# Performance work log

Hardware: AMD Instinct MI355X
Metric: run time of the kernel (lower is better)

## Reference

```python
import jax, jax.numpy as jnp
import numpy as np

B, T, C = 1, 4096, 1024
NH, NKV, HD = 16, 4, 64
N_REP = NH // NKV
WIN = 1024
EPS = 1e-5
ROPE_THETA = 10000.0


def setup_inputs() -> dict:
    key = jax.random.key(0)
    ks = jax.random.split(key, 6)
    s = 1.0 / np.sqrt(C)
    x = jax.random.normal(ks[0], (B, T, C), jnp.float32)
    wq = jax.random.normal(ks[1], (NH * HD, C), jnp.float32) * s
    wk = jax.random.normal(ks[2], (NKV * HD, C), jnp.float32) * s
    wv = jax.random.normal(ks[3], (NKV * HD, C), jnp.float32) * s
    wo = jax.random.normal(ks[4], (C, NH * HD), jnp.float32) * (1.0 / np.sqrt(NH * HD))
    q_norm_w = jnp.ones((HD,), jnp.float32)
    k_norm_w = jnp.ones((HD,), jnp.float32)
    # RoPE tables: (T, HD//2)
    inv_freq = 1.0 / (ROPE_THETA ** (np.arange(0, HD, 2, dtype=np.float32) / HD))
    ang = np.outer(np.arange(T, dtype=np.float32), inv_freq)
    freqs_cos = jnp.asarray(np.cos(ang), jnp.float32)
    freqs_sin = jnp.asarray(np.sin(ang), jnp.float32)
    return {"x": x, "wq": wq, "wk": wk, "wv": wv, "wo": wo,
            "q_norm_w": q_norm_w, "k_norm_w": k_norm_w,
            "freqs_cos": freqs_cos, "freqs_sin": freqs_sin}


def _rmsnorm(v, w):
    # RMSNorm over last dim (per-head)
    return v * jax.lax.rsqrt(jnp.mean(v * v, axis=-1, keepdims=True) + EPS) * w


def _rope(v, cos, sin):
    # v: (B, T, H, HD); interleaved complex rotation, matching torch polar freqs_cis
    vr, vi = v[..., 0::2], v[..., 1::2]
    c = cos[None, :, None, :]
    s = sin[None, :, None, :]
    out_r = vr * c - vi * s
    out_i = vr * s + vi * c
    return jnp.stack([out_r, out_i], axis=-1).reshape(v.shape)


def reference(x, wq, wk, wv, wo, q_norm_w, k_norm_w, freqs_cos, freqs_sin):
    xq = jnp.einsum('btc,dc->btd', x, wq).reshape(B, T, NH, HD)
    xk = jnp.einsum('btc,dc->btd', x, wk).reshape(B, T, NKV, HD)
    xv = jnp.einsum('btc,dc->btd', x, wv).reshape(B, T, NKV, HD)
    # per-head QK RMSNorm
    xq = _rmsnorm(xq, q_norm_w)
    xk = _rmsnorm(xk, k_norm_w)
    # RoPE
    xq = _rope(xq, freqs_cos, freqs_sin)
    xk = _rope(xk, freqs_cos, freqs_sin)
    # GQA: expand kv heads
    xk = jnp.repeat(xk, N_REP, axis=2)  # (B, T, NH, HD)
    xv = jnp.repeat(xv, N_REP, axis=2)
    scale = 1.0 / np.sqrt(HD)
    scores = jnp.einsum('bthd,bshd->bhts', xq, xk) * scale
    i = jnp.arange(T)[:, None]
    j = jnp.arange(T)[None, :]
    mask = (i >= j) & (i - j < WIN)  # causal + sliding window
    scores = jnp.where(mask[None, None], scores, -jnp.inf)
    attn = jax.nn.softmax(scores, axis=-1)
    y = jnp.einsum('bhts,bshd->bthd', attn, xv).reshape(B, T, NH * HD)
    return jnp.einsum('btd,cd->btc', y, wo)
```

## Files before the change

### kernel.cpp

```cpp
#include <hip/hip_runtime.h>
#include <hip/hip_bf16.h>


#define WIN_SZ 1024

typedef __attribute__((ext_vector_type(8))) short short8;
typedef __attribute__((ext_vector_type(8))) unsigned short ushort8;
typedef __attribute__((ext_vector_type(4))) float f32x4;
typedef __attribute__((ext_vector_type(16))) float f32x16;

#define GLOAD_LDS16(g, s)                                              \
  __builtin_amdgcn_global_load_lds(                                    \
      (const __attribute__((address_space(1))) unsigned int*)(g),      \
      (__attribute__((address_space(3))) unsigned int*)(s), 16, 0, 0)

__device__ __forceinline__ unsigned short f2bf(float f) {
  union { float f; unsigned u; } v; v.f = f;
  unsigned r = v.u + 0x7fffu + ((v.u >> 16) & 1u);
  return (unsigned short)(r >> 16);
}

__device__ __forceinline__ unsigned pk2bf(float lo, float hi) {
  __hip_bfloat162 h = __float22bfloat162_rn(make_float2(lo, hi));
  union { __hip_bfloat162 h; unsigned u; } c; c.h = h; return c.u;
}

__device__ __forceinline__ short8 frag4(unsigned w0, unsigned w1, unsigned w2, unsigned w3) {
  union { unsigned u[4]; short8 s; } x;
  x.u[0] = w0; x.u[1] = w1; x.u[2] = w2; x.u[3] = w3; return x.s;
}

__global__ __launch_bounds__(256) void k_f2b_all(const float* __restrict__ x,
                                                 const float* __restrict__ wq,
                                                 const float* __restrict__ wk,
                                                 const float* __restrict__ wv,
                                                 const float* __restrict__ wo,
                                                 unsigned short* __restrict__ xb,
                                                 unsigned short* __restrict__ wqkvb,
                                                 unsigned short* __restrict__ wob) {
  int q = blockIdx.x * 256 + threadIdx.x;
  const float* src;
  unsigned short* dst;
  int off;
  if (q < 1048576) { src = x; dst = xb; off = q; }
  else if (q < 1310720) { src = wq; dst = wqkvb; off = q - 1048576; }
  else if (q < 1376256) { src = wk; dst = wqkvb + 1024 * 1024; off = q - 1310720; }
  else if (q < 1441792) { src = wv; dst = wqkvb + 1280 * 1024; off = q - 1376256; }
  else { src = wo; dst = wob; off = q - 1441792; }
  float4 v = ((const float4*)src)[off];
  ushort4 o;
  o.x = f2bf(v.x); o.y = f2bf(v.y); o.z = f2bf(v.z); o.w = f2bf(v.w);
  ((ushort4*)dst)[off] = o;
}

__global__ __launch_bounds__(256) void k_gemm_qkv(const unsigned short* __restrict__ A,
                                                  const unsigned short* __restrict__ B,
                                                  const float* __restrict__ qw,
                                                  const float* __restrict__ kw,
                                                  const float* __restrict__ fc,
                                                  const float* __restrict__ fs,
                                                  unsigned short* __restrict__ Qb,
                                                  unsigned short* __restrict__ Kb,
                                                  unsigned short* __restrict__ Vtg) {
  const int K = 1024;
  __shared__ unsigned short As[2][128 * 64];
  __shared__ unsigned short Bs[2][64 * 64];
  const int id = blockIdx.x;
  const int chunk = gridDim.x >> 3;
  const int swz = (id & 7) * chunk + (id >> 3);
  const int n_idx = swz % 24, m_idx = swz / 24;
  const int m0 = m_idx * 128, n0 = n_idx * 64;

  const int tid = threadIdx.x;
  const int w = tid >> 6, l = tid & 63;
  const int wr = w >> 1, wc = w & 1;
  const int r = l & 15, g = l >> 4;
  const int lr = l >> 3, lc = l & 7;
  const int srowb = w * 32, browb = w * 16;

  f32x4 acc[4][2];
#pragma unroll
  for (int i = 0; i < 4; i++)
#pragma unroll
    for (int j = 0; j < 2; j++) acc[i][j] = {0.f, 0.f, 0.f, 0.f};

  const unsigned short* Ag = A + (size_t)(m0 + srowb + lr) * K + lc * 8;
  const unsigned short* Bg = B + (size_t)(n0 + browb + lr) * K + lc * 8;

  auto stage = [&](int buf, int k0) {
#pragma unroll
    for (int it = 0; it < 4; it++)
      GLOAD_LDS16(Ag + (size_t)(it * 8) * K + k0, &As[buf][(srowb + it * 8) * 64]);
#pragma unroll
    for (int it = 0; it < 2; it++)
      GLOAD_LDS16(Bg + (size_t)(it * 8) * K + k0, &Bs[buf][(browb + it * 8) * 64]);
  };

  stage(0, 0);
  __syncthreads();
  int cur = 0;
  const int NT = K >> 6;
  for (int t = 0; t < NT; ++t) {
    if (t + 1 < NT) stage(cur ^ 1, (t + 1) << 6);
    const char* Ab = (const char*)As[cur];
    const char* Bb = (const char*)Bs[cur];
#pragma unroll
    for (int kk = 0; kk < 2; kk++) {
      short8 af[4], bfr[2];
#pragma unroll
      for (int mi = 0; mi < 4; mi++)
        af[mi] = *(const short8*)(Ab + (wr * 64 + mi * 16 + r) * 128 + kk * 64 + g * 16);
#pragma unroll
      for (int nj = 0; nj < 2; nj++)
        bfr[nj] = *(const short8*)(Bb + (wc * 32 + nj * 16 + r) * 128 + kk * 64 + g * 16);
#pragma unroll
      for (int mi = 0; mi < 4; mi++)
#pragma unroll
        for (int nj = 0; nj < 2; nj++)
          acc[mi][nj] = __builtin_amdgcn_mfma_f32_16x16x32_bf16(af[mi], bfr[nj], acc[mi][nj], 0, 0, 0);
    }
    __syncthreads();
    cur ^= 1;
  }

  const int u = n0 >> 6;
  if (u < 20) {
    float* ssb = (float*)As;
    f32x4 sv[4];
#pragma unroll
    for (int mi = 0; mi < 4; mi++) {
      f32x4 s;
#pragma unroll
      for (int e = 0; e < 4; e++)
        s[e] = acc[mi][0][e] * acc[mi][0][e] + acc[mi][1][e] * acc[mi][1][e];
#pragma unroll
      for (int off = 1; off < 16; off <<= 1)
#pragma unroll
        for (int e = 0; e < 4; e++) s[e] += __shfl_xor(s[e], off);
      sv[mi] = s;
    }
    if (r == 0) {
#pragma unroll
      for (int mi = 0; mi < 4; mi++)
#pragma unroll
        for (int e = 0; e < 4; e++)
          ssb[(wr * 64 + mi * 16 + g * 4 + e) * 2 + wc] = sv[mi][e];
    }
    __syncthreads();
    const float escale = (u < 16) ? 0.1803368801111204f : 1.0f;
    const float* wgt = (u < 16) ? qw : kw;
#pragma unroll
    for (int mi = 0; mi < 4; mi++) {
      const int rl0 = wr * 64 + mi * 16 + g * 4;
      const int row0 = m0 + rl0;
#pragma unroll
      for (int e = 0; e < 4; e++) {
        const int row = row0 + e;
        float ss = ssb[(rl0 + e) * 2] + ssb[(rl0 + e) * 2 + 1];
        float rms = rsqrtf(ss * (1.0f / 64.0f) + 1e-5f);
#pragma unroll
        for (int nj = 0; nj < 2; nj++) {
          const int cl = wc * 32 + nj * 16 + r;
          float vn = acc[mi][nj][e] * rms * wgt[cl];
          float c = fc[row * 32 + (cl >> 1)];
          float s = fs[row * 32 + (cl >> 1)];
          float pvn = __shfl_xor(vn, 1);
          float outv = (cl & 1) ? (pvn * s + vn * c) : (vn * c - pvn * s);
          unsigned short ob = f2bf(outv * escale);
          if (u < 16) Qb[(size_t)row * 1024 + n0 + cl] = ob;
          else Kb[(size_t)row * 256 + (n0 - 1024) + cl] = ob;
        }
      }
    }
  } else {
#pragma unroll
    for (int mi = 0; mi < 4; mi++) {
      const int row0 = m0 + wr * 64 + mi * 16 + g * 4;
#pragma unroll
      for (int nj = 0; nj < 2; nj++) {
        const int d = (n0 - 1280) + wc * 32 + nj * 16 + r;
        ushort4 ov;
        ov.x = f2bf(acc[mi][nj][0]);
        ov.y = f2bf(acc[mi][nj][1]);
        ov.z = f2bf(acc[mi][nj][2]);
        ov.w = f2bf(acc[mi][nj][3]);
        *(ushort4*)(Vtg + (size_t)d * 4096 + row0) = ov;
      }
    }
  }
}

__global__ __launch_bounds__(256) void k_gemm_out(const unsigned short* __restrict__ A,
                                                  const unsigned short* __restrict__ B,
                                                  float* __restrict__ C) {
  const int K = 1024, N = 1024;
  __shared__ unsigned short As[2][128 * 64];
  __shared__ unsigned short Bs[2][64 * 64];
  const int id = blockIdx.x;
  const int chunk = gridDim.x >> 3;
  const int swz = (id & 7) * chunk + (id >> 3);
  const int n_idx = swz % 16, m_idx = swz / 16;
  const int m0 = m_idx * 128, n0 = n_idx * 64;

  const int tid = threadIdx.x;
  const int w = tid >> 6, l = tid & 63;
  const int wr = w >> 1, wc = w & 1;
  const int r = l & 15, g = l >> 4;
  const int lr = l >> 3, lc = l & 7;
  const int srowb = w * 32, browb = w * 16;

  f32x4 acc[4][2];
#pragma unroll
  for (int i = 0; i < 4; i++)
#pragma unroll
    for (int j = 0; j < 2; j++) acc[i][j] = {0.f, 0.f, 0.f, 0.f};

  const unsigned short* Ag = A + (size_t)(m0 + srowb + lr) * K + lc * 8;
  const unsigned short* Bg = B + (size_t)(n0 + browb + lr) * K + lc * 8;

  auto stage = [&](int buf, int k0) {
#pragma unroll
    for (int it = 0; it < 4; it++)
      GLOAD_LDS16(Ag + (size_t)(it * 8) * K + k0, &As[buf][(srowb + it * 8) * 64]);
#pragma unroll
    for (int it = 0; it < 2; it++)
      GLOAD_LDS16(Bg + (size_t)(it * 8) * K + k0, &Bs[buf][(browb + it * 8) * 64]);
  };

  stage(0, 0);
  __syncthreads();
  int cur = 0;
  const int NT = K >> 6;
  for (int t = 0; t < NT; ++t) {
    if (t + 1 < NT) stage(cur ^ 1, (t + 1) << 6);
    const char* Ab = (const char*)As[cur];
    const char* Bb = (const char*)Bs[cur];
#pragma unroll
    for (int kk = 0; kk < 2; kk++) {
      short8 af[4], bfr[2];
#pragma unroll
      for (int mi = 0; mi < 4; mi++)
        af[mi] = *(const short8*)(Ab + (wr * 64 + mi * 16 + r) * 128 + kk * 64 + g * 16);
#pragma unroll
      for (int nj = 0; nj < 2; nj++)
        bfr[nj] = *(const short8*)(Bb + (wc * 32 + nj * 16 + r) * 128 + kk * 64 + g * 16);
#pragma unroll
      for (int mi = 0; mi < 4; mi++)
#pragma unroll
        for (int nj = 0; nj < 2; nj++)
          acc[mi][nj] = __builtin_amdgcn_mfma_f32_16x16x32_bf16(af[mi], bfr[nj], acc[mi][nj], 0, 0, 0);
    }
    __syncthreads();
    cur ^= 1;
  }

#pragma unroll
  for (int mi = 0; mi < 4; mi++)
#pragma unroll
    for (int nj = 0; nj < 2; nj++) {
      int row = m0 + wr * 64 + mi * 16 + g * 4;
      int col = n0 + wc * 32 + nj * 16 + r;
#pragma unroll
      for (int e = 0; e < 4; e++)
        C[(size_t)(row + e) * N + col] = acc[mi][nj][e];
    }
}

__global__ __launch_bounds__(512, 4) void k_attn9(const unsigned short* __restrict__ Qb,
                                                  const unsigned short* __restrict__ Kb,
                                                  const unsigned short* __restrict__ Vtg,
                                                  unsigned short* __restrict__ Yb) {
  __shared__ char smem[4 * 8192 + 1024];
  char* stage = smem;
  float* Obuf = (float*)smem;
  float* ml = (float*)(smem + 32768);

  const int id = blockIdx.x;
  const int cupair = id & 255, sel = id >> 8;
  int qi = cupair >> 1;
  if (sel) qi = 127 - qi;
  const int hk = (cupair & 1) * 2 + sel;
  const int q0 = qi * 32;

  const int tid = threadIdx.x, w = tid >> 6, l = tid & 63;
  const int hh = w & 3, half = w >> 2;
  const int h = hk * 4 + hh;
  const int l31 = l & 31, hi = l >> 5, l15 = l & 15;
  const int qrow = q0 + l31;

  int jlo = q0 - (WIN_SZ - 1);
  if (jlo < 0) jlo = 0;
  jlo &= ~63;
  const int jlast = ((q0 + 31) >> 6) << 6;
  const int nt = ((jlast - jlo) >> 6) + 1;
  const int nh0 = (nt + 1) >> 1;

  const int sb = tid >> 7;
  const int su = tid & 127;
  const int srow = su >> 1;
  const int sg = (su & 1) * 4;
  const int sbase = sb * 8192 + (srow & 31) * 256;
  const int srx = (srow & 15) << 4;
  const int srh = (srow >> 5) * 128;
  const bool isV = sb & 1;
  const unsigned short* gK = Kb + (size_t)srow * 256 + hk * 64 + sg * 8;
  const unsigned short* gV = Vtg + (size_t)(hk * 64 + srow) * 4096 + sg * 8;

  short8 qf[4];
#pragma unroll
  for (int ks = 0; ks < 4; ks++)
    qf[ks] = *(const short8*)(Qb + (size_t)qrow * 1024 + h * 64 + ks * 16 + hi * 8);

  const short8 ones = frag4(0x3F803F80u, 0x3F803F80u, 0x3F803F80u, 0x3F803F80u);

  f32x16 accO0, accO1;
#pragma unroll
  for (int i = 0; i < 16; i++) { accO0[i] = 0.f; accO1[i] = 0.f; }
  float m = -1e30f, lsum = 0.f;

  ushort8 pre[4];
  auto prefetch = [&](int s) {
    int jt0 = jlo + (s << 6);
    int t1 = nh0 + s;
    int jt1 = (t1 < nt) ? (jlo + (t1 << 6)) : jlo;
    int jt = (sb >= 2) ? jt1 : jt0;
    if (!isV) {
      const unsigned short* g = gK + (size_t)jt * 256;
#pragma unroll
      for (int e = 0; e < 4; e++) pre[e] = *(const ushort8*)(g + e * 8);
    } else {
      const unsigned short* g = gV + jt;
#pragma unroll
      for (int e = 0; e < 4; e++) pre[e] = *(const ushort8*)(g + e * 8);
    }
  };
  prefetch(0);

  const int kbase = half * 16384;
  const int vbase = kbase + 8192;

  for (int s = 0; s < nh0; ++s) {
    __syncthreads();
#pragma unroll
    for (int e = 0; e < 4; e++) {
      int dst = sbase + ((srh + (sg + e) * 16) ^ srx);
      *(ushort8*)(stage + dst) = pre[e];
    }
    __syncthreads();
    if (s + 1 < nh0) prefetch(s + 1);

    const int myt = half ? (nh0 + s) : s;
    if (myt < nt) {
      const int jt = jlo + (myt << 6);

      f32x16 st0, st1;
#pragma unroll
      for (int i = 0; i < 16; i++) { st0[i] = 0.f; st1[i] = 0.f; }
      __builtin_amdgcn_s_setprio(1);
#pragma unroll
      for (int ks = 0; ks < 4; ks++) {
        int colb = ks * 32 + hi * 16;
        short8 kf0 = *(const short8*)(stage + kbase + l31 * 256 + (colb ^ (l15 << 4)));
        st0 = __builtin_amdgcn_mfma_f32_32x32x16_bf16(kf0, qf[ks], st0, 0, 0, 0);
        short8 kf1 = *(const short8*)(stage + kbase + l31 * 256 + ((128 + colb) ^ (l15 << 4)));
        st1 = __builtin_amdgcn_mfma_f32_32x32x16_bf16(kf1, qf[ks], st1, 0, 0, 0);
      }
      __builtin_amdgcn_s_setprio(0);

      if (jt + 63 > q0 || (q0 + 31) - jt >= WIN_SZ) {
        const int jb = jt + hi * 4;
#pragma unroll
        for (int rg = 0; rg < 16; rg++) {
          int j0 = jb + (rg & 3) + 8 * (rg >> 2);
          if (!((j0 <= qrow) && (qrow - j0 < WIN_SZ))) st0[rg] = -3.0e38f;
          int j1 = j0 + 32;
          if (!((j1 <= qrow) && (qrow - j1 < WIN_SZ))) st1[rg] = -3.0e38f;
        }
      }

      float mx = st0[0];
#pragma unroll
      for (int rg = 1; rg < 16; rg++) mx = fmaxf(mx, st0[rg]);
#pragma unroll
      for (int rg = 0; rg < 16; rg++) mx = fmaxf(mx, st1[rg]);
      mx = fmaxf(mx, __shfl_xor(mx, 32));
      if (!__all(mx <= m + 8.0f)) {
        float mnew = fmaxf(m, mx);
        float alpha = exp2f(m - mnew);
#pragma unroll
        for (int rg = 0; rg < 16; rg++) { accO0[rg] *= alpha; accO1[rg] *= alpha; }
        lsum *= alpha;
        m = mnew;
      }
#pragma unroll
      for (int rg = 0; rg < 16; rg++) st0[rg] = exp2f(st0[rg] - m);
#pragma unroll
      for (int rg = 0; rg < 16; rg++) st1[rg] = exp2f(st1[rg] - m);

      unsigned pd0[2][4], pd1[2][4];
#pragma unroll
      for (int b = 0; b < 4; b++) {
        pd0[0][b] = pk2bf(st0[4 * b], st0[4 * b + 1]);
        pd1[0][b] = pk2bf(st0[4 * b + 2], st0[4 * b + 3]);
        pd0[1][b] = pk2bf(st1[4 * b], st1[4 * b + 1]);
        pd1[1][b] = pk2bf(st1[4 * b + 2], st1[4 * b + 3]);
      }

      f32x16 accL;
#pragma unroll
      for (int i = 0; i < 16; i++) accL[i] = 0.f;

      __builtin_amdgcn_s_setprio(1);
#pragma unroll
      for (int jj = 0; jj < 2; jj++) {
#pragma unroll
        for (int ks2 = 0; ks2 < 2; ks2++) {
          unsigned a0 = pd0[jj][2 * ks2], a1 = pd0[jj][2 * ks2 + 1];
          unsigned b0 = pd1[jj][2 * ks2], b1 = pd1[jj][2 * ks2 + 1];
          unsigned a0x = __shfl_xor(a0, 32), a1x = __shfl_xor(a1, 32);
          unsigned b0x = __shfl_xor(b0, 32), b1x = __shfl_xor(b1, 32);
          unsigned w0 = hi ? a1x : a0;
          unsigned w1 = hi ? b1x : b0;
          unsigned w2 = hi ? a1 : a0x;
          unsigned w3 = hi ? b1 : b0x;
          short8 pf = frag4(w0, w1, w2, w3);
          int colb2 = jj * 64 + ks2 * 32 + hi * 16;
          short8 vf0 = *(const short8*)(stage + vbase + l31 * 256 + (colb2 ^ (l15 << 4)));
          accO0 = __builtin_amdgcn_mfma_f32_32x32x16_bf16(vf0, pf, accO0, 0, 0, 0);
          short8 vf1 = *(const short8*)(stage + vbase + l31 * 256 + ((128 + colb2) ^ (l15 << 4)));
          accO1 = __builtin_amdgcn_mfma_f32_32x32x16_bf16(vf1, pf, accO1, 0, 0, 0);
          accL = __builtin_amdgcn_mfma_f32_32x32x16_bf16(ones, pf, accL, 0, 0, 0);
        }
      }
      __builtin_amdgcn_s_setprio(0);
      lsum += accL[0];
    }
  }

  __syncthreads();
  if (half == 1) {
#pragma unroll
    for (int dd = 0; dd < 2; dd++) {
      const f32x16& a = dd ? accO1 : accO0;
#pragma unroll
      for (int rg = 0; rg < 16; rg++) {
        int d = dd * 32 + 8 * (rg >> 2) + 4 * hi + (rg & 3);
        Obuf[(hh * 64 + d) * 32 + l31] = a[rg];
      }
    }
    if (!hi) { ml[(hh * 2 + 0) * 32 + l31] = m; ml[(hh * 2 + 1) * 32 + l31] = lsum; }
  }
  __syncthreads();
  if (half == 0) {
    float m1 = ml[(hh * 2 + 0) * 32 + l31];
    float l1 = ml[(hh * 2 + 1) * 32 + l31];
    float ms = fmaxf(m, m1);
    float a0 = exp2f(m - ms), a1 = exp2f(m1 - ms);
    float inv = 1.0f / (lsum * a0 + l1 * a1);
    a0 *= inv; a1 *= inv;
#pragma unroll
    for (int dd = 0; dd < 2; dd++) {
      const f32x16& a = dd ? accO1 : accO0;
#pragma unroll
      for (int b = 0; b < 4; b++) {
        float o[4];
#pragma unroll
        for (int e = 0; e < 4; e++) {
          int d = dd * 32 + 8 * b + 4 * hi + e;
          o[e] = a[4 * b + e] * a0 + Obuf[(hh * 64 + d) * 32 + l31] * a1;
        }
        union { unsigned uu[2]; ushort4 v; } ov;
        ov.uu[0] = pk2bf(o[0], o[1]);
        ov.uu[1] = pk2bf(o[2], o[3]);
        *(ushort4*)(Yb + (size_t)qrow * 1024 + h * 64 + dd * 32 + b * 8 + hi * 4) = ov.v;
      }
    }
  }
}

extern "C" void kernel_launch(void* const* d_in, const int* in_sizes, int n_in,
                              void* d_out, int out_size, void* d_ws, size_t ws_size,
                              hipStream_t stream) {
  const float* x = (const float*)d_in[0];
  const float* wq = (const float*)d_in[1];
  const float* wk = (const float*)d_in[2];
  const float* wv = (const float*)d_in[3];
  const float* wo = (const float*)d_in[4];
  const float* qw = (const float*)d_in[5];
  const float* kw = (const float*)d_in[6];
  const float* fc = (const float*)d_in[7];
  const float* fs = (const float*)d_in[8];
  float* out = (float*)d_out;

  char* p = (char*)d_ws;
  auto alloc = [&](size_t b) {
    char* q = p;
    p += (b + 255) & ~(size_t)255;
    return q;
  };
  unsigned short* xb = (unsigned short*)alloc((size_t)4096 * 1024 * 2);
  unsigned short* wqkvb = (unsigned short*)alloc((size_t)1536 * 1024 * 2);
  unsigned short* wob = (unsigned short*)alloc((size_t)1024 * 1024 * 2);
  unsigned short* Qb = (unsigned short*)alloc((size_t)4096 * 1024 * 2);
  unsigned short* Kb = (unsigned short*)alloc((size_t)4096 * 256 * 2);
  unsigned short* Vtg = (unsigned short*)alloc((size_t)256 * 4096 * 2);
  unsigned short* Yb = (unsigned short*)alloc((size_t)4096 * 1024 * 2);

  k_f2b_all<<<6656, 256, 0, stream>>>(x, wq, wk, wv, wo, xb, wqkvb, wob);
  k_gemm_qkv<<<768, 256, 0, stream>>>(xb, wqkvb, qw, kw, fc, fs, Qb, Kb, Vtg);
  k_attn9<<<512, 512, 0, stream>>>(Qb, Kb, Vtg, Yb);
  k_gemm_out<<<512, 256, 0, stream>>>(Yb, wob, out);
}
```

Baseline: 108.8 us.

## Stage two K/V tiles per barrier pair in sliding-window attention kernel

The attention kernel now stages two 64-key K/V tiles per half-block into shared memory at once (LDS doubled to 64KB+), so each barrier-separated iteration processes two tiles and the outer loop runs half as many times. Each thread now loads a full 64-element row (8 vectors) instead of 4, which halves the count of __syncthreads and global prefetch rounds per tile. This costs more registers for the prefetch buffer and more LDS per block, which may lower occupancy given launch bounds of 4 blocks of 512 threads.

```diff
diff --git a/kernel.cpp b/kernel.cpp
--- a/kernel.cpp
+++ b/kernel.cpp
@@ -266,14 +266,14 @@
     }
 }
 
-__global__ __launch_bounds__(512, 4) void k_attn9(const unsigned short* __restrict__ Qb,
-                                                  const unsigned short* __restrict__ Kb,
-                                                  const unsigned short* __restrict__ Vtg,
-                                                  unsigned short* __restrict__ Yb) {
-  __shared__ char smem[4 * 8192 + 1024];
+__global__ __launch_bounds__(512, 4) void k_attn10(const unsigned short* __restrict__ Qb,
+                                                   const unsigned short* __restrict__ Kb,
+                                                   const unsigned short* __restrict__ Vtg,
+                                                   unsigned short* __restrict__ Yb) {
+  __shared__ char smem[8 * 8192 + 1024];
   char* stage = smem;
   float* Obuf = (float*)smem;
-  float* ml = (float*)(smem + 32768);
+  float* ml = (float*)(smem + 65536);
 
   const int id = blockIdx.x;
   const int cupair = id & 255, sel = id >> 8;
@@ -294,17 +294,18 @@
   const int jlast = ((q0 + 31) >> 6) << 6;
   const int nt = ((jlast - jlo) >> 6) + 1;
   const int nh0 = (nt + 1) >> 1;
-
-  const int sb = tid >> 7;
-  const int su = tid & 127;
-  const int srow = su >> 1;
-  const int sg = (su & 1) * 4;
+  const int S = (nh0 + 1) >> 1;
+
+  const int sb = tid >> 6;
+  const int sq = sb >> 2;
+  const int sp = (sb >> 1) & 1;
+  const bool isV = sb & 1;
+  const int srow = tid & 63;
   const int sbase = sb * 8192 + (srow & 31) * 256;
   const int srx = (srow & 15) << 4;
   const int srh = (srow >> 5) * 128;
-  const bool isV = sb & 1;
-  const unsigned short* gK = Kb + (size_t)srow * 256 + hk * 64 + sg * 8;
-  const unsigned short* gV = Vtg + (size_t)(hk * 64 + srow) * 4096 + sg * 8;
+  const unsigned short* gK = Kb + (size_t)srow * 256 + hk * 64;
+  const unsigned short* gV = Vtg + (size_t)(hk * 64 + srow) * 4096;
 
   short8 qf[4];
 #pragma unroll
@@ -318,122 +319,126 @@
   for (int i = 0; i < 16; i++) { accO0[i] = 0.f; accO1[i] = 0.f; }
   float m = -1e30f, lsum = 0.f;
 
-  ushort8 pre[4];
+  ushort8 pre[8];
   auto prefetch = [&](int s) {
-    int jt0 = jlo + (s << 6);
-    int t1 = nh0 + s;
-    int jt1 = (t1 < nt) ? (jlo + (t1 << 6)) : jlo;
-    int jt = (sb >= 2) ? jt1 : jt0;
+    int t = (sq ? nh0 : 0) + 2 * s + sp;
+    int lim = sq ? nt : nh0;
+    int jt = (t < lim) ? (jlo + (t << 6)) : jlo;
     if (!isV) {
       const unsigned short* g = gK + (size_t)jt * 256;
 #pragma unroll
-      for (int e = 0; e < 4; e++) pre[e] = *(const ushort8*)(g + e * 8);
+      for (int e = 0; e < 8; e++) pre[e] = *(const ushort8*)(g + e * 8);
     } else {
       const unsigned short* g = gV + jt;
 #pragma unroll
-      for (int e = 0; e < 4; e++) pre[e] = *(const ushort8*)(g + e * 8);
+      for (int e = 0; e < 8; e++) pre[e] = *(const ushort8*)(g + e * 8);
     }
   };
   prefetch(0);
 
-  const int kbase = half * 16384;
-  const int vbase = kbase + 8192;
-
-  for (int s = 0; s < nh0; ++s) {
+  const int tbase = half ? nh0 : 0;
+  const int tlim = half ? nt : nh0;
+
+  for (int s = 0; s < S; ++s) {
     __syncthreads();
 #pragma unroll
-    for (int e = 0; e < 4; e++) {
-      int dst = sbase + ((srh + (sg + e) * 16) ^ srx);
+    for (int e = 0; e < 8; e++) {
+      int dst = sbase + ((srh + e * 16) ^ srx);
       *(ushort8*)(stage + dst) = pre[e];
     }
     __syncthreads();
-    if (s + 1 < nh0) prefetch(s + 1);
-
-    const int myt = half ? (nh0 + s) : s;
-    if (myt < nt) {
-      const int jt = jlo + (myt << 6);
-
-      f32x16 st0, st1;
-#pragma unroll
-      for (int i = 0; i < 16; i++) { st0[i] = 0.f; st1[i] = 0.f; }
-      __builtin_amdgcn_s_setprio(1);
-#pragma unroll
-      for (int ks = 0; ks < 4; ks++) {
-        int colb = ks * 32 + hi * 16;
-        short8 kf0 = *(const short8*)(stage + kbase + l31 * 256 + (colb ^ (l15 << 4)));
-        st0 = __builtin_amdgcn_mfma_f32_32x32x16_bf16(kf0, qf[ks], st0, 0, 0, 0);
-        short8 kf1 = *(const short8*)(stage + kbase + l31 * 256 + ((128 + colb) ^ (l15 << 4)));
-        st1 = __builtin_amdgcn_mfma_f32_32x32x16_bf16(kf1, qf[ks], st1, 0, 0, 0);
+    if (s + 1 < S) prefetch(s + 1);
+
+#pragma unroll
+    for (int p = 0; p < 2; ++p) {
+      const int myt = tbase + 2 * s + p;
+      if (myt < tlim) {
+        const int jt = jlo + (myt << 6);
+        const int kbase = (half * 4 + p * 2) * 8192;
+        const int vbase = kbase + 8192;
+
+        f32x16 st0, st1;
+#pragma unroll
+        for (int i = 0; i < 16; i++) { st0[i] = 0.f; st1[i] = 0.f; }
+        __builtin_amdgcn_s_setprio(1);
+#pragma unroll
+        for (int ks = 0; ks < 4; ks++) {
+          int colb = ks * 32 + hi * 16;
+          short8 kf0 = *(const short8*)(stage + kbase + l31 * 256 + (colb ^ (l15 << 4)));
+          st0 = __builtin_amdgcn_mfma_f32_32x32x16_bf16(kf0, qf[ks], st0, 0, 0, 0);
+          short8 kf1 = *(const short8*)(stage + kbase + l31 * 256 + ((128 + colb) ^ (l15 << 4)));
+          st1 = __builtin_amdgcn_mfma_f32_32x32x16_bf16(kf1, qf[ks], st1, 0, 0, 0);
+        }
+        __builtin_amdgcn_s_setprio(0);
+
+        if (jt + 63 > q0 || (q0 + 31) - jt >= WIN_SZ) {
+          const int jb = jt + hi * 4;
+#pragma unroll
+          for (int rg = 0; rg < 16; rg++) {
+            int j0 = jb + (rg & 3) + 8 * (rg >> 2);
+            if (!((j0 <= qrow) && (qrow - j0 < WIN_SZ))) st0[rg] = -3.0e38f;
+            int j1 = j0 + 32;
+            if (!((j1 <= qrow) && (qrow - j1 < WIN_SZ))) st1[rg] = -3.0e38f;
+          }
+        }
+
+        float mx = st0[0];
+#pragma unroll
+        for (int rg = 1; rg < 16; rg++) mx = fmaxf(mx, st0[rg]);
+#pragma unroll
+        for (int rg = 0; rg < 16; rg++) mx = fmaxf(mx, st1[rg]);
+        mx = fmaxf(mx, __shfl_xor(mx, 32));
+        if (!__all(mx <= m + 8.0f)) {
+          float mnew = fmaxf(m, mx);
+          float alpha = exp2f(m - mnew);
+#pragma unroll
+          for (int rg = 0; rg < 16; rg++) { accO0[rg] *= alpha; accO1[rg] *= alpha; }
+          lsum *= alpha;
+          m = mnew;
+        }
+#pragma unroll
+        for (int rg = 0; rg < 16; rg++) st0[rg] = exp2f(st0[rg] - m);
+#pragma unroll
+        for (int rg = 0; rg < 16; rg++) st1[rg] = exp2f(st1[rg] - m);
+
+        unsigned pd0[2][4], pd1[2][4];
+#pragma unroll
+        for (int b = 0; b < 4; b++) {
+          pd0[0][b] = pk2bf(st0[4 * b], st0[4 * b + 1]);
+          pd1[0][b] = pk2bf(st0[4 * b + 2], st0[4 * b + 3]);
+          pd0[1][b] = pk2bf(st1[4 * b], st1[4 * b + 1]);
+          pd1[1][b] = pk2bf(st1[4 * b + 2], st1[4 * b + 3]);
+        }
+
+        f32x16 accL;
+#pragma unroll
+        for (int i = 0; i < 16; i++) accL[i] = 0.f;
+
+        __builtin_amdgcn_s_setprio(1);
+#pragma unroll
+        for (int jj = 0; jj < 2; jj++) {
+#pragma unroll
+          for (int ks2 = 0; ks2 < 2; ks2++) {
+            unsigned a0 = pd0[jj][2 * ks2], a1 = pd0[jj][2 * ks2 + 1];
+            unsigned b0 = pd1[jj][2 * ks2], b1 = pd1[jj][2 * ks2 + 1];
+            unsigned a0x = __shfl_xor(a0, 32), a1x = __shfl_xor(a1, 32);
+            unsigned b0x = __shfl_xor(b0, 32), b1x = __shfl_xor(b1, 32);
+            unsigned w0 = hi ? a1x : a0;
+            unsigned w1 = hi ? b1x : b0;
+            unsigned w2 = hi ? a1 : a0x;
+            unsigned w3 = hi ? b1 : b0x;
+            short8 pf = frag4(w0, w1, w2, w3);
+            int colb2 = jj * 64 + ks2 * 32 + hi * 16;
+            short8 vf0 = *(const short8*)(stage + vbase + l31 * 256 + (colb2 ^ (l15 << 4)));
+            accO0 = __builtin_amdgcn_mfma_f32_32x32x16_bf16(vf0, pf, accO0, 0, 0, 0);
+            short8 vf1 = *(const short8*)(stage + vbase + l31 * 256 + ((128 + colb2) ^ (l15 << 4)));
+            accO1 = __builtin_amdgcn_mfma_f32_32x32x16_bf16(vf1, pf, accO1, 0, 0, 0);
+            accL = __builtin_amdgcn_mfma_f32_32x32x16_bf16(ones, pf, accL, 0, 0, 0);
+          }
+        }
+        __builtin_amdgcn_s_setprio(0);
+        lsum += accL[0];
       }
-      __builtin_amdgcn_s_setprio(0);
-
-      if (jt + 63 > q0 || (q0 + 31) - jt >= WIN_SZ) {
-        const int jb = jt + hi * 4;
-#pragma unroll
-        for (int rg = 0; rg < 16; rg++) {
-          int j0 = jb + (rg & 3) + 8 * (rg >> 2);
-          if (!((j0 <= qrow) && (qrow - j0 < WIN_SZ))) st0[rg] = -3.0e38f;
-          int j1 = j0 + 32;
-          if (!((j1 <= qrow) && (qrow - j1 < WIN_SZ))) st1[rg] = -3.0e38f;
-        }
-      }
-
-      float mx = st0[0];
-#pragma unroll
-      for (int rg = 1; rg < 16; rg++) mx = fmaxf(mx, st0[rg]);
-#pragma unroll
-      for (int rg = 0; rg < 16; rg++) mx = fmaxf(mx, st1[rg]);
-      mx = fmaxf(mx, __shfl_xor(mx, 32));
-      if (!__all(mx <= m + 8.0f)) {
-        float mnew = fmaxf(m, mx);
-        float alpha = exp2f(m - mnew);
-#pragma unroll
-        for (int rg = 0; rg < 16; rg++) { accO0[rg] *= alpha; accO1[rg] *= alpha; }
-        lsum *= alpha;
-        m = mnew;
-      }
-#pragma unroll
-      for (int rg = 0; rg < 16; rg++) st0[rg] = exp2f(st0[rg] - m);
-#pragma unroll
-      for (int rg = 0; rg < 16; rg++) st1[rg] = exp2f(st1[rg] - m);
-
-      unsigned pd0[2][4], pd1[2][4];
-#pragma unroll
-      for (int b = 0; b < 4; b++) {
-        pd0[0][b] = pk2bf(st0[4 * b], st0[4 * b + 1]);
-        pd1[0][b] = pk2bf(st0[4 * b + 2], st0[4 * b + 3]);
-        pd0[1][b] = pk2bf(st1[4 * b], st1[4 * b + 1]);
-        pd1[1][b] = pk2bf(st1[4 * b + 2], st1[4 * b + 3]);
-      }
-
-      f32x16 accL;
-#pragma unroll
-      for (int i = 0; i < 16; i++) accL[i] = 0.f;
-
-      __builtin_amdgcn_s_setprio(1);
-#pragma unroll
-      for (int jj = 0; jj < 2; jj++) {
-#pragma unroll
-        for (int ks2 = 0; ks2 < 2; ks2++) {
-          unsigned a0 = pd0[jj][2 * ks2], a1 = pd0[jj][2 * ks2 + 1];
-          unsigned b0 = pd1[jj][2 * ks2], b1 = pd1[jj][2 * ks2 + 1];
-          unsigned a0x = __shfl_xor(a0, 32), a1x = __shfl_xor(a1, 32);
-          unsigned b0x = __shfl_xor(b0, 32), b1x = __shfl_xor(b1, 32);
-          unsigned w0 = hi ? a1x : a0;
-          unsigned w1 = hi ? b1x : b0;
-          unsigned w2 = hi ? a1 : a0x;
-          unsigned w3 = hi ? b1 : b0x;
-          short8 pf = frag4(w0, w1, w2, w3);
-          int colb2 = jj * 64 + ks2 * 32 + hi * 16;
-          short8 vf0 = *(const short8*)(stage + vbase + l31 * 256 + (colb2 ^ (l15 << 4)));
-          accO0 = __builtin_amdgcn_mfma_f32_32x32x16_bf16(vf0, pf, accO0, 0, 0, 0);
-          short8 vf1 = *(const short8*)(stage + vbase + l31 * 256 + ((128 + colb2) ^ (l15 << 4)));
-          accO1 = __builtin_amdgcn_mfma_f32_32x32x16_bf16(vf1, pf, accO1, 0, 0, 0);
-          accL = __builtin_amdgcn_mfma_f32_32x32x16_bf16(ones, pf, accL, 0, 0, 0);
-        }
-      }
-      __builtin_amdgcn_s_setprio(0);
-      lsum += accL[0];
     }
   }
 
@@ -508,6 +513,6 @@
 
   k_f2b_all<<<6656, 256, 0, stream>>>(x, wq, wk, wv, wo, xb, wqkvb, wob);
   k_gemm_qkv<<<768, 256, 0, stream>>>(xb, wqkvb, qw, kw, fc, fs, Qb, Kb, Vtg);
-  k_attn9<<<512, 512, 0, stream>>>(Qb, Kb, Vtg, Yb);
+  k_attn10<<<512, 512, 0, stream>>>(Qb, Kb, Vtg, Yb);
   k_gemm_out<<<512, 256, 0, stream>>>(Yb, wob, out);
 }
```

Result: slower. 145.5 us (+33.8%).
